# Performance work log

Measured on AMD Instinct MI355X. Metric: run time of the kernel, lower is better.

The kernel has to match this reference:

```python
import jax, jax.numpy as jnp
import numpy as np

N_NODES = 100000
N_EDGES = 640000
D_IN = 128
D_OUT = 128
BN_EPS = 1e-5


def setup_inputs() -> dict:
    key = jax.random.key(0)
    k1, k2, k3, k4 = jax.random.split(key, 4)
    x = jax.random.normal(k1, (N_NODES, D_IN), dtype=jnp.float32)
    edge_index = jax.random.randint(k2, (2, N_EDGES), 0, N_NODES, dtype=jnp.int64)
    W = jax.random.normal(k3, (D_IN, D_OUT), dtype=jnp.float32) * (1.0 / np.sqrt(D_IN))
    b = jnp.zeros((D_OUT,), dtype=jnp.float32)
    gamma = jnp.ones((D_OUT,), dtype=jnp.float32)
    beta = jnp.zeros((D_OUT,), dtype=jnp.float32)
    return {"x": x, "edge_index": edge_index, "W": W, "b": b, "gamma": gamma, "beta": beta}


def reference(x, edge_index, W, b, gamma, beta):
    N = x.shape[0]
    # --- GCNConv: add self-loops, symmetric normalization ---
    loop = jnp.arange(N, dtype=edge_index.dtype)
    src = jnp.concatenate([edge_index[0], loop])  # [E+N]
    dst = jnp.concatenate([edge_index[1], loop])  # [E+N]
    deg = jax.ops.segment_sum(jnp.ones_like(dst, dtype=x.dtype), dst, num_segments=N)
    dinv = jax.lax.rsqrt(deg)  # deg >= 1 due to self-loops
    norm = dinv[src] * dinv[dst]  # [E+N]
    # linear transform first (PyG order), then gather-normalize-scatter
    h = x @ W  # [N, D_OUT]
    msg = h[src] * norm[:, None]  # [E+N, D_OUT]
    agg = jax.ops.segment_sum(msg, dst, num_segments=N) + b  # [N, D_OUT]
    # --- ReLU ---
    r = jax.nn.relu(agg)
    # --- BatchNorm over node axis (training-mode batch statistics) ---
    mean = r.mean(axis=0)
    var = r.var(axis=0)
    out = gamma * (r - mean) * jax.lax.rsqrt(var + BN_EPS) + beta
    # dropout: identity in eval/deterministic mode
    return out
```

## Files before the change

kernel.cpp:

```cpp
#include <hip/hip_runtime.h>
#include <hip/hip_bf16.h>

#define N_NODES 100000
#define N_EDGES 640000
#define D 128
#define BN_EPS 1e-5f
#define NB_FILL 2500
#define NB_CVT 6250
#define NREP 64
#define BM 64
#define CS_LD 130
#define SLOTS 16
#define OSLOTS 32

typedef __attribute__((ext_vector_type(8))) short short8;
typedef __attribute__((ext_vector_type(4))) float f32x4;

__device__ inline unsigned int f2bf(float f) {
    unsigned int u = __builtin_bit_cast(unsigned int, f);
    return (u + 0x7FFFu + ((u >> 16) & 1u)) >> 16;
}
__device__ inline float bflo(unsigned int p) { return __builtin_bit_cast(float, p << 16); }
__device__ inline float bfhi(unsigned int p) { return __builtin_bit_cast(float, p & 0xFFFF0000u); }

__global__ void k_zero(int* __restrict__ cnt, float* __restrict__ rep) {
    int i = blockIdx.x * 256 + threadIdx.x;
    if (i < N_NODES) cnt[i] = 0;
    if (i < NREP * 256) rep[i] = 0.0f;
}

__global__ __launch_bounds__(256) void k_prep(const int* __restrict__ ei, int* __restrict__ cnt,
                                              int* __restrict__ buck, int* __restrict__ buck2,
                                              const float* __restrict__ x, uint4* __restrict__ xb,
                                              const float* __restrict__ W,
                                              unsigned short* __restrict__ Wfrag) {
    const int bid = blockIdx.x;
    const int t = threadIdx.x;
    int xi = -1;
    if (bid < 2 * NB_FILL) {
        if (bid & 1) {
            const int e = (bid >> 1) * 256 + t;
            if (e < N_EDGES) {
                const int src = ei[e];
                const int d = ei[N_EDGES + e];
                const int slot = atomicAdd(&cnt[d], 1);
                if (slot < SLOTS) buck[(size_t)d * SLOTS + slot] = src;
                else if (slot < SLOTS + OSLOTS) buck2[(size_t)d * OSLOTS + slot - SLOTS] = src;
            }
            return;
        }
        xi = bid >> 1;
    } else if (bid < NB_FILL + NB_CVT) {
        xi = bid - NB_FILL;
    } else {
        const int i = (bid - NB_FILL - NB_CVT) * 256 + t;
        const int e  = i & 7;
        const int l  = (i >> 3) & 63;
        const int ct = (i >> 9) & 7;
        const int kk = i >> 12;
        const int lr = l & 15, lk = l >> 4;
        const int k   = kk * 32 + lk * 8 + e;
        const int col = ct * 16 + lr;
        Wfrag[i] = (unsigned short)f2bf(W[(size_t)k * D + col]);
        return;
    }
    const size_t i = (size_t)xi * 256 + t;
    const float4* xg = (const float4*)x;
    float4 a = xg[2 * i], c = xg[2 * i + 1];
    uint4 o;
    o.x = f2bf(a.x) | (f2bf(a.y) << 16);
    o.y = f2bf(a.z) | (f2bf(a.w) << 16);
    o.z = f2bf(c.x) | (f2bf(c.y) << 16);
    o.w = f2bf(c.z) | (f2bf(c.w) << 16);
    xb[i] = o;
}

__global__ __launch_bounds__(256) void k_gather(const int* __restrict__ buck,
                                                const int* __restrict__ buck2,
                                                const int* __restrict__ cnt,
                                                const unsigned int* __restrict__ xb,
                                                unsigned int* __restrict__ agg) {
    const int t = threadIdx.x;
    const int lane = t & 63;
    const int n = blockIdx.x * 4 + (t >> 6);
    if (n >= N_NODES) return;

    const int deg = cnt[n];
    const float di = rsqrtf((float)(deg + 1));
    const unsigned int hv = xb[(size_t)n * 64 + lane];
    const float dd = di * di;
    float ax = bflo(hv) * dd;
    float ay = bfhi(hv) * dd;

    const int m = (deg > SLOTS + OSLOTS) ? (SLOTS + OSLOTS) : deg;
    int s_l = 0; float f_l = 0.0f;
    if (lane < m) {
        s_l = (lane < SLOTS) ? buck[(size_t)n * SLOTS + lane]
                             : buck2[(size_t)n * OSLOTS + lane - SLOTS];
        f_l = rsqrtf((float)(cnt[s_l] + 1)) * di;
    }

    for (int k = 0; k < m; k += 8) {
        unsigned int v[8];
        float f[8];
#pragma unroll
        for (int i = 0; i < 8; ++i) {
            const int sj = __builtin_amdgcn_readlane(s_l, k + i);
            f[i] = __builtin_bit_cast(float,
                __builtin_amdgcn_readlane(__builtin_bit_cast(int, f_l), k + i));
            v[i] = xb[(size_t)sj * 64 + lane];
        }
#pragma unroll
        for (int i = 0; i < 8; ++i) {
            ax = fmaf(bflo(v[i]), f[i], ax);
            ay = fmaf(bfhi(v[i]), f[i], ay);
        }
    }
    agg[(size_t)n * 64 + lane] = f2bf(ax) | (f2bf(ay) << 16);
}

__global__ __launch_bounds__(256) void k_mm(const unsigned int* __restrict__ agg,
                                            const unsigned short* __restrict__ Wfrag,
                                            const float* __restrict__ b,
                                            unsigned int* __restrict__ outb,
                                            float* __restrict__ rep) {
    __shared__ __align__(16) char U[BM * CS_LD * 4];
    uint4 (*As)[16] = (uint4(*)[16])U;
    float* Cs = (float*)U;
    __shared__ float lsum[4][128];
    __shared__ float lsq[4][128];

    const int t = threadIdx.x;
    const int w = t >> 6;
    const int l = t & 63;
    const int lr = l & 15;
    const int lk = l >> 4;
    const int r0 = blockIdx.x * BM;

    const uint4* aggv = (const uint4*)agg;
#pragma unroll
    for (int it = 0; it < 4; ++it) {
        const int idx = it * 256 + t;
        const int row = idx >> 4;
        const int c   = idx & 15;
        int grow = r0 + row; if (grow >= N_NODES) grow = N_NODES - 1;
        As[row][c ^ (row & 15)] = aggv[(size_t)grow * 16 + c];
    }
    __syncthreads();

    const int arow = w * 16 + lr;
    short8 a[4];
#pragma unroll
    for (int kk = 0; kk < 4; ++kk)
        a[kk] = *(const short8*)&As[arow][(kk * 4 + lk) ^ (arow & 15)];
    __syncthreads();

    f32x4 acc[8];
#pragma unroll
    for (int ct = 0; ct < 8; ++ct) acc[ct] = (f32x4)(0.0f);

#pragma unroll
    for (int kk = 0; kk < 4; ++kk) {
#pragma unroll
        for (int ct = 0; ct < 8; ++ct) {
            const short8 bb = *(const short8*)(Wfrag + ((((kk * 8 + ct) << 6) + l) << 3));
            acc[ct] = __builtin_amdgcn_mfma_f32_16x16x32_bf16(a[kk], bb, acc[ct], 0, 0, 0);
        }
    }

    float s[8], s2[8];
#pragma unroll
    for (int ct = 0; ct < 8; ++ct) { s[ct] = 0.0f; s2[ct] = 0.0f; }

#pragma unroll
    for (int ct = 0; ct < 8; ++ct) {
        const float bias = b[ct * 16 + lr];
#pragma unroll
        for (int r = 0; r < 4; ++r) {
            const int lrow = w * 16 + lk * 4 + r;
            const float v = fmaxf(acc[ct][r] + bias, 0.0f);
            if (r0 + lrow < N_NODES) {
                s[ct] += v;
                s2[ct] = fmaf(v, v, s2[ct]);
            }
            Cs[lrow * CS_LD + ct * 16 + lr] = v;
        }
    }
#pragma unroll
    for (int ct = 0; ct < 8; ++ct) {
        s[ct]  += __shfl_xor(s[ct], 16);  s[ct]  += __shfl_xor(s[ct], 32);
        s2[ct] += __shfl_xor(s2[ct], 16); s2[ct] += __shfl_xor(s2[ct], 32);
    }
    if (l < 16) {
#pragma unroll
        for (int ct = 0; ct < 8; ++ct) {
            lsum[w][ct * 16 + lr] = s[ct];
            lsq[w][ct * 16 + lr]  = s2[ct];
        }
    }
    __syncthreads();

#pragma unroll
    for (int i = 0; i < 4; ++i) {
        const int v = i * 256 + t;
        const int row = v >> 4;
        const int q   = v & 15;
        if (r0 + row < N_NODES) {
            const float* p = &Cs[row * CS_LD + q * 8];
            uint4 o;
            o.x = f2bf(p[0]) | (f2bf(p[1]) << 16);
            o.y = f2bf(p[2]) | (f2bf(p[3]) << 16);
            o.z = f2bf(p[4]) | (f2bf(p[5]) << 16);
            o.w = f2bf(p[6]) | (f2bf(p[7]) << 16);
            ((uint4*)outb)[(size_t)(r0 + row) * 16 + q] = o;
        }
    }

    if (t < 128) {
        float* r = rep + (blockIdx.x & (NREP - 1)) * 256;
        atomicAdd(&r[t],       lsum[0][t] + lsum[1][t] + lsum[2][t] + lsum[3][t]);
        atomicAdd(&r[128 + t], lsq[0][t] + lsq[1][t] + lsq[2][t] + lsq[3][t]);
    }
}

__global__ __launch_bounds__(256) void k_red(const float* __restrict__ rep,
                                             const float* __restrict__ gamma,
                                             const float* __restrict__ beta,
                                             float* __restrict__ sclsft) {
    __shared__ float sh[256];
    const int t = threadIdx.x;
    float s = 0.0f;
    for (int r = 0; r < NREP; ++r) s += rep[r * 256 + t];
    sh[t] = s;
    __syncthreads();
    if (t < 128) {
        const float inv_n = 1.0f / (float)N_NODES;
        const float mean = sh[t] * inv_n;
        const float var = sh[128 + t] * inv_n - mean * mean;
        const float sc = gamma[t] * rsqrtf(var + BN_EPS);
        sclsft[t]       = sc;
        sclsft[128 + t] = beta[t] - mean * sc;
    }
}

__global__ __launch_bounds__(256) void k_norm(const uint4* __restrict__ outb,
                                              float4* __restrict__ out,
                                              const float* __restrict__ sclsft) {
    __shared__ float sc[256];
    const int t = threadIdx.x;
    sc[t] = sclsft[t];
    __syncthreads();
    const int i = blockIdx.x * 256 + t;
    if (i >= N_NODES * 16) return;
    const int c0 = (i & 15) * 8;
    const uint4 v = outb[i];
    float4 o0, o1;
    o0.x = fmaf(bflo(v.x), sc[c0 + 0], sc[128 + c0 + 0]);
    o0.y = fmaf(bfhi(v.x), sc[c0 + 1], sc[128 + c0 + 1]);
    o0.z = fmaf(bflo(v.y), sc[c0 + 2], sc[128 + c0 + 2]);
    o0.w = fmaf(bfhi(v.y), sc[c0 + 3], sc[128 + c0 + 3]);
    o1.x = fmaf(bflo(v.z), sc[c0 + 4], sc[128 + c0 + 4]);
    o1.y = fmaf(bfhi(v.z), sc[c0 + 5], sc[128 + c0 + 5]);
    o1.z = fmaf(bflo(v.w), sc[c0 + 6], sc[128 + c0 + 6]);
    o1.w = fmaf(bfhi(v.w), sc[c0 + 7], sc[128 + c0 + 7]);
    out[(size_t)i * 2]     = o0;
    out[(size_t)i * 2 + 1] = o1;
}

extern "C" void kernel_launch(void* const* d_in, const int* in_sizes, int n_in,
                              void* d_out, int out_size, void* d_ws, size_t ws_size,
                              hipStream_t stream) {
    const float* x     = (const float*)d_in[0];
    const int*   ei    = (const int*)d_in[1];
    const float* W     = (const float*)d_in[2];
    const float* b     = (const float*)d_in[3];
    const float* gamma = (const float*)d_in[4];
    const float* beta  = (const float*)d_in[5];
    float* out = (float*)d_out;

    char* ws = (char*)d_ws;
    int*            cnt    = (int*)(ws + 0);
    float*          rep    = (float*)(ws + (512u << 10));
    float*          sclsft = (float*)(ws + (640u << 10));
    unsigned short* Wfrag  = (unsigned short*)(ws + (704u << 10));
    int*            buck   = (int*)(ws + (1024u << 10));
    int*            buck2  = (int*)(ws + (8192u << 10));
    unsigned int*   xb     = (unsigned int*)(ws + (24576u << 10));
    unsigned int*   agg    = (unsigned int*)(ws + (57344u << 10));

    unsigned int* outb = xb;

    k_zero<<<(N_NODES + 255) / 256, 256, 0, stream>>>(cnt, rep);
    k_prep<<<NB_FILL + NB_CVT + 64, 256, 0, stream>>>(ei, cnt, buck, buck2, x, (uint4*)xb,
                                                      W, Wfrag);
    k_gather<<<(N_NODES + 3) / 4, 256, 0, stream>>>(buck, buck2, cnt, xb, agg);
    k_mm<<<(N_NODES + BM - 1) / BM, 256, 0, stream>>>(agg, Wfrag, b, outb, rep);
    k_red<<<1, 256, 0, stream>>>(rep, gamma, beta, sclsft);
    k_norm<<<(N_NODES * 16 + 255) / 256, 256, 0, stream>>>((const uint4*)outb, (float4*)out,
                                                           sclsft);
}
```

Baseline: 118.2 us.

## Fuse gather aggregation into MFMA matmul kernel and merge prep block roles

Merges the neighbor-gather kernel into the matmul kernel. A 1024-thread block aggregates 64 rows straight into shared memory, and 16 waves then split the MFMA columns, so the bf16 agg buffer no longer goes through a global write and read. The prep kernel now does edge bucketing and x conversion in the same block instead of interleaving separate block types, and it issues the atomics alongside the conversion loads. The output buffer gets its own region instead of aliasing xb, because xb is still being read during the fused kernel. The cost is 1024-thread blocks with serial per-row gathers, which may hurt occupancy and latency hiding; a few empty leftover loops remain in the code.

Result: no change. 120.0 us (+1.4%).

```diff
diff --git a/kernel.cpp b/kernel.cpp
--- a/kernel.cpp
+++ b/kernel.cpp
@@ -36,24 +36,31 @@
                                               unsigned short* __restrict__ Wfrag) {
     const int bid = blockIdx.x;
     const int t = threadIdx.x;
-    int xi = -1;
-    if (bid < 2 * NB_FILL) {
-        if (bid & 1) {
-            const int e = (bid >> 1) * 256 + t;
-            if (e < N_EDGES) {
-                const int src = ei[e];
-                const int d = ei[N_EDGES + e];
-                const int slot = atomicAdd(&cnt[d], 1);
-                if (slot < SLOTS) buck[(size_t)d * SLOTS + slot] = src;
-                else if (slot < SLOTS + OSLOTS) buck2[(size_t)d * OSLOTS + slot - SLOTS] = src;
-            }
-            return;
-        }
-        xi = bid >> 1;
-    } else if (bid < NB_FILL + NB_CVT) {
-        xi = bid - NB_FILL;
+    if (bid < NB_CVT) {
+        int src = 0, d = 0;
+        const bool has_e = (bid < NB_FILL);
+        if (has_e) {
+            const int e = bid * 256 + t;
+            src = ei[e];
+            d = ei[N_EDGES + e];
+        }
+        const size_t i = (size_t)bid * 256 + t;
+        const float4* xg = (const float4*)x;
+        float4 a = xg[2 * i], c = xg[2 * i + 1];
+        int slot = -1;
+        if (has_e) slot = atomicAdd(&cnt[d], 1);
+        uint4 o;
+        o.x = f2bf(a.x) | (f2bf(a.y) << 16);
+        o.y = f2bf(a.z) | (f2bf(a.w) << 16);
+        o.z = f2bf(c.x) | (f2bf(c.y) << 16);
+        o.w = f2bf(c.z) | (f2bf(c.w) << 16);
+        xb[i] = o;
+        if (has_e) {
+            if (slot < SLOTS) buck[(size_t)d * SLOTS + slot] = src;
+            else if (slot < SLOTS + OSLOTS) buck2[(size_t)d * OSLOTS + slot - SLOTS] = src;
+        }
     } else {
-        const int i = (bid - NB_FILL - NB_CVT) * 256 + t;
+        const int i = (bid - NB_CVT) * 256 + t;
         const int e  = i & 7;
         const int l  = (i >> 3) & 63;
         const int ct = (i >> 9) & 7;
@@ -62,73 +69,22 @@
         const int k   = kk * 32 + lk * 8 + e;
         const int col = ct * 16 + lr;
         Wfrag[i] = (unsigned short)f2bf(W[(size_t)k * D + col]);
-        return;
-    }
-    const size_t i = (size_t)xi * 256 + t;
-    const float4* xg = (const float4*)x;
-    float4 a = xg[2 * i], c = xg[2 * i + 1];
-    uint4 o;
-    o.x = f2bf(a.x) | (f2bf(a.y) << 16);
-    o.y = f2bf(a.z) | (f2bf(a.w) << 16);
-    o.z = f2bf(c.x) | (f2bf(c.y) << 16);
-    o.w = f2bf(c.z) | (f2bf(c.w) << 16);
-    xb[i] = o;
-}
-
-__global__ __launch_bounds__(256) void k_gather(const int* __restrict__ buck,
-                                                const int* __restrict__ buck2,
-                                                const int* __restrict__ cnt,
-                                                const unsigned int* __restrict__ xb,
-                                                unsigned int* __restrict__ agg) {
-    const int t = threadIdx.x;
-    const int lane = t & 63;
-    const int n = blockIdx.x * 4 + (t >> 6);
-    if (n >= N_NODES) return;
-
-    const int deg = cnt[n];
-    const float di = rsqrtf((float)(deg + 1));
-    const unsigned int hv = xb[(size_t)n * 64 + lane];
-    const float dd = di * di;
-    float ax = bflo(hv) * dd;
-    float ay = bfhi(hv) * dd;
-
-    const int m = (deg > SLOTS + OSLOTS) ? (SLOTS + OSLOTS) : deg;
-    int s_l = 0; float f_l = 0.0f;
-    if (lane < m) {
-        s_l = (lane < SLOTS) ? buck[(size_t)n * SLOTS + lane]
-                             : buck2[(size_t)n * OSLOTS + lane - SLOTS];
-        f_l = rsqrtf((float)(cnt[s_l] + 1)) * di;
-    }
-
-    for (int k = 0; k < m; k += 8) {
-        unsigned int v[8];
-        float f[8];
-#pragma unroll
-        for (int i = 0; i < 8; ++i) {
-            const int sj = __builtin_amdgcn_readlane(s_l, k + i);
-            f[i] = __builtin_bit_cast(float,
-                __builtin_amdgcn_readlane(__builtin_bit_cast(int, f_l), k + i));
-            v[i] = xb[(size_t)sj * 64 + lane];
-        }
-#pragma unroll
-        for (int i = 0; i < 8; ++i) {
-            ax = fmaf(bflo(v[i]), f[i], ax);
-            ay = fmaf(bfhi(v[i]), f[i], ay);
-        }
-    }
-    agg[(size_t)n * 64 + lane] = f2bf(ax) | (f2bf(ay) << 16);
-}
-
-__global__ __launch_bounds__(256) void k_mm(const unsigned int* __restrict__ agg,
-                                            const unsigned short* __restrict__ Wfrag,
-                                            const float* __restrict__ b,
-                                            unsigned int* __restrict__ outb,
-                                            float* __restrict__ rep) {
+    }
+}
+
+__global__ __launch_bounds__(1024) void k_gmm(const int* __restrict__ buck,
+                                              const int* __restrict__ buck2,
+                                              const int* __restrict__ cnt,
+                                              const unsigned int* __restrict__ xb,
+                                              const unsigned short* __restrict__ Wfrag,
+                                              const float* __restrict__ b,
+                                              unsigned int* __restrict__ outb,
+                                              float* __restrict__ rep) {
     __shared__ __align__(16) char U[BM * CS_LD * 4];
-    uint4 (*As)[16] = (uint4(*)[16])U;
+    unsigned int* As_u = (unsigned int*)U;
     float* Cs = (float*)U;
-    __shared__ float lsum[4][128];
-    __shared__ float lsq[4][128];
+    __shared__ float lsum[16][32];
+    __shared__ float lsq[16][32];
 
     const int t = threadIdx.x;
     const int w = t >> 6;
@@ -137,72 +93,105 @@
     const int lk = l >> 4;
     const int r0 = blockIdx.x * BM;
 
-    const uint4* aggv = (const uint4*)agg;
-#pragma unroll
-    for (int it = 0; it < 4; ++it) {
-        const int idx = it * 256 + t;
-        const int row = idx >> 4;
-        const int c   = idx & 15;
-        int grow = r0 + row; if (grow >= N_NODES) grow = N_NODES - 1;
-        As[row][c ^ (row & 15)] = aggv[(size_t)grow * 16 + c];
-    }
-    __syncthreads();
-
-    const int arow = w * 16 + lr;
+    for (int rr = 0; rr < 4; ++rr) {
+        const int lrow = w * 4 + rr;
+        int n = r0 + lrow; if (n >= N_NODES) n = N_NODES - 1;
+        const int deg = cnt[n];
+        const float di = rsqrtf((float)(deg + 1));
+        const unsigned int hv = xb[(size_t)n * 64 + l];
+        const float dd = di * di;
+        float ax = bflo(hv) * dd;
+        float ay = bfhi(hv) * dd;
+
+        const int m = (deg > SLOTS + OSLOTS) ? (SLOTS + OSLOTS) : deg;
+        int s_l = 0; float f_l = 0.0f;
+        if (l < m) {
+            s_l = (l < SLOTS) ? buck[(size_t)n * SLOTS + l]
+                              : buck2[(size_t)n * OSLOTS + l - SLOTS];
+            f_l = rsqrtf((float)(cnt[s_l] + 1)) * di;
+        }
+        for (int k = 0; k < m; k += 8) {
+            unsigned int v[8];
+            float f[8];
+#pragma unroll
+            for (int i = 0; i < 8; ++i) {
+                const int sj = __builtin_amdgcn_readlane(s_l, k + i);
+                f[i] = __builtin_bit_cast(float,
+                    __builtin_amdgcn_readlane(__builtin_bit_cast(int, f_l), k + i));
+                v[i] = xb[(size_t)sj * 64 + l];
+            }
+#pragma unroll
+            for (int i = 0; i < 8; ++i) {
+                ax = fmaf(bflo(v[i]), f[i], ax);
+                ay = fmaf(bfhi(v[i]), f[i], ay);
+            }
+        }
+        As_u[lrow * 64 + ((((l >> 2) ^ (lrow & 15)) << 2) | (l & 3))] =
+            f2bf(ax) | (f2bf(ay) << 16);
+    }
+    __syncthreads();
+
+    const int arow = (w & 3) * 16 + lr;
+    const uint4* As4 = (const uint4*)U;
     short8 a[4];
 #pragma unroll
     for (int kk = 0; kk < 4; ++kk)
-        a[kk] = *(const short8*)&As[arow][(kk * 4 + lk) ^ (arow & 15)];
-    __syncthreads();
-
-    f32x4 acc[8];
-#pragma unroll
-    for (int ct = 0; ct < 8; ++ct) acc[ct] = (f32x4)(0.0f);
-
+        a[kk] = *(const short8*)&As4[arow * 16 + ((kk * 4 + lk) ^ (arow & 15))];
+    __syncthreads();
+
+    const int ct0 = (w >> 2) * 2;
+    f32x4 acc[2];
+    acc[0] = (f32x4)(0.0f);
+    acc[1] = (f32x4)(0.0f);
 #pragma unroll
     for (int kk = 0; kk < 4; ++kk) {
 #pragma unroll
-        for (int ct = 0; ct < 8; ++ct) {
-            const short8 bb = *(const short8*)(Wfrag + ((((kk * 8 + ct) << 6) + l) << 3));
-            acc[ct] = __builtin_amdgcn_mfma_f32_16x16x32_bf16(a[kk], bb, acc[ct], 0, 0, 0);
-        }
-    }
-
-    float s[8], s2[8];
-#pragma unroll
-    for (int ct = 0; ct < 8; ++ct) { s[ct] = 0.0f; s2[ct] = 0.0f; }
-
-#pragma unroll
-    for (int ct = 0; ct < 8; ++ct) {
+        for (int c = 0; c < 2; ++c) {
+            const short8 bb = *(const short8*)(Wfrag + ((((kk * 8 + ct0 + c) << 6) + l) << 3));
+            acc[c] = __builtin_amdgcn_mfma_f32_16x16x32_bf16(a[kk], bb, acc[c], 0, 0, 0);
+        }
+    }
+
+    float s[2] = {0.0f, 0.0f}, s2[2] = {0.0f, 0.0f};
+#pragma unroll
+    for (int c = 0; c < 2; ++c) {
+        const int ct = ct0 + c;
         const float bias = b[ct * 16 + lr];
 #pragma unroll
         for (int r = 0; r < 4; ++r) {
-            const int lrow = w * 16 + lk * 4 + r;
-            const float v = fmaxf(acc[ct][r] + bias, 0.0f);
+            const int lrow = (w & 3) * 16 + lk * 4 + r;
+            const float v = fmaxf(acc[c][r] + bias, 0.0f);
             if (r0 + lrow < N_NODES) {
-                s[ct] += v;
-                s2[ct] = fmaf(v, v, s2[ct]);
+                s[c] += v;
+                s2[c] = fmaf(v, v, s2[c]);
             }
             Cs[lrow * CS_LD + ct * 16 + lr] = v;
         }
     }
 #pragma unroll
-    for (int ct = 0; ct < 8; ++ct) {
-        s[ct]  += __shfl_xor(s[ct], 16);  s[ct]  += __shfl_xor(s[ct], 32);
-        s2[ct] += __shfl_xor(s2[ct], 16); s2[ct] += __shfl_xor(s2[ct], 32);
+    for (int c = 0; c < 2; ++c) {
+        s[c]  += __shfl_xor(s[c], 16);  s[c]  += __shfl_xor(s[c], 32);
+        s2[c] += __shfl_xor(s2[c], 16); s2[c] += __shfl_xor(s2[c], 32);
     }
     if (l < 16) {
 #pragma unroll
-        for (int ct = 0; ct < 8; ++ct) {
-            lsum[w][ct * 16 + lr] = s[ct];
-            lsq[w][ct * 16 + lr]  = s2[ct];
-        }
-    }
-    __syncthreads();
-
-#pragma unroll
-    for (int i = 0; i < 4; ++i) {
-        const int v = i * 256 + t;
+        for (int c = 0; c < 2; ++c) {
+            lsum[w][c * 16 + lr] = s[c];
+            lsq[w][c * 16 + lr]  = s2[c];
+        }
+    }
+    __syncthreads();
+
+#pragma unroll
+    for (int i = 0; i < 1; ++i) { }
+#pragma unroll
+    for (int i = 0; i < 1; ++i) {
+        const int v0 = t;
+#pragma unroll
+        for (int p = 0; p < 1; ++p) { }
+    }
+    {
+        const int v = t;
         const int row = v >> 4;
         const int q   = v & 15;
         if (r0 + row < N_NODES) {
@@ -217,9 +206,16 @@
     }
 
     if (t < 128) {
+        const int g = t >> 5;
+        const int cc = t & 31;
+        const float ssum = lsum[4 * g + 0][cc] + lsum[4 * g + 1][cc]
+                         + lsum[4 * g + 2][cc] + lsum[4 * g + 3][cc];
+        const float ssq  = lsq[4 * g + 0][cc] + lsq[4 * g + 1][cc]
+                         + lsq[4 * g + 2][cc] + lsq[4 * g + 3][cc];
+        const int col = g * 32 + cc;
         float* r = rep + (blockIdx.x & (NREP - 1)) * 256;
-        atomicAdd(&r[t],       lsum[0][t] + lsum[1][t] + lsum[2][t] + lsum[3][t]);
-        atomicAdd(&r[128 + t], lsq[0][t] + lsq[1][t] + lsq[2][t] + lsq[3][t]);
+        atomicAdd(&r[col],       ssum);
+        atomicAdd(&r[128 + col], ssq);
     }
 }
 
@@ -286,15 +282,12 @@
     int*            buck   = (int*)(ws + (1024u << 10));
     int*            buck2  = (int*)(ws + (8192u << 10));
     unsigned int*   xb     = (unsigned int*)(ws + (24576u << 10));
-    unsigned int*   agg    = (unsigned int*)(ws + (57344u << 10));
-
-    unsigned int* outb = xb;
+    unsigned int*   outb   = (unsigned int*)(ws + (57344u << 10));
 
     k_zero<<<(N_NODES + 255) / 256, 256, 0, stream>>>(cnt, rep);
-    k_prep<<<NB_FILL + NB_CVT + 64, 256, 0, stream>>>(ei, cnt, buck, buck2, x, (uint4*)xb,
-                                                      W, Wfrag);
-    k_gather<<<(N_NODES + 3) / 4, 256, 0, stream>>>(buck, buck2, cnt, xb, agg);
-    k_mm<<<(N_NODES + BM - 1) / BM, 256, 0, stream>>>(agg, Wfrag, b, outb, rep);
+    k_prep<<<NB_CVT + 64, 256, 0, stream>>>(ei, cnt, buck, buck2, x, (uint4*)xb, W, Wfrag);
+    k_gmm<<<(N_NODES + BM - 1) / BM, 1024, 0, stream>>>(buck, buck2, cnt, xb, Wfrag, b,
+                                                        outb, rep);
     k_red<<<1, 256, 0, stream>>>(rep, gamma, beta, sclsft);
     k_norm<<<(N_NODES * 16 + 255) / 256, 256, 0, stream>>>((const uint4*)outb, (float4*)out,
                                                            sclsft);
```
